# Optimization experiments

Measured on AMD Instinct MI355X. Metric: run time of the kernel, lower is better.

Reference implementation:

```python
import jax, jax.numpy as jnp
import numpy as np

T, H, E, I, K = 1024, 2048, 32, 1024, 2  # tokens, hidden, experts, intermediate (per rank), top_k


def setup_inputs() -> dict:
    key = jax.random.key(0)
    k0, k1, k2, k3 = jax.random.split(key, 4)
    s = 0.02  # weight init scale
    return {
        "hidden_states": jax.random.normal(k0, (T, H), jnp.float32),
        "w_qkv": jax.random.normal(k1, (3 * E, H), jnp.float32) * s,   # router query_key_value weight
        "w1": jax.random.normal(k2, (E, 2 * I, H), jnp.float32) * s,   # gate/up projection per expert
        "w2": jax.random.normal(k3, (E, H, I), jnp.float32) * s,       # down projection per expert
    }


def _router_logits(x, w_qkv):
    # ParallelAttention_router: per-token attention over the expert axis.
    mix = x @ w_qkv.T                      # [T, 3E]
    q, k, v = jnp.split(mix, 3, axis=-1)   # each [T, E]
    q = q.astype(jnp.float32)
    k = k.astype(jnp.float32)
    v = v.astype(jnp.float32)
    # attn[t, e, f] = softmax_f(q[t, e] * k[t, f])
    attn = jax.nn.softmax(q[:, :, None] * k[:, None, :], axis=-1)  # [T, E, E]
    return jnp.einsum('tef,tf->te', attn, v)                        # [T, E]


def reference(hidden_states, w_qkv, w1, w2):
    n_tok = hidden_states.shape[0]
    logits = _router_logits(hidden_states, w_qkv)                   # [T, E]
    top_logits, topk_ids = jax.lax.top_k(logits, K)                 # [T, K]
    topk_w = jax.nn.softmax(top_logits.astype(jnp.float32), axis=-1)  # renormalize=False -> plain softmax over top-k
    # Dense combine weights: zero for non-selected experts (honors top-k sparsity in math).
    combine = jnp.zeros((n_tok, E), jnp.float32).at[
        jnp.arange(n_tok)[:, None], topk_ids].add(topk_w)           # [T, E]
    # Expert MLP: SiLU-gated FFN (fused_experts contract: w1 -> [gate; up], w2 -> down).
    gate_up = jnp.einsum('th,eih->tei', hidden_states, w1)          # [T, E, 2I]
    gate, up = jnp.split(gate_up, 2, axis=-1)                       # each [T, E, I]
    h = jax.nn.silu(gate) * up * combine[:, :, None]                # fold combine weight in early
    out = jnp.einsum('tei,ehi->th', h, w2)                          # [T, H]
    return out.astype(hidden_states.dtype)
```

## Files before the change

kernel.cpp:

```cpp
#include <hip/hip_runtime.h>
#include <hip/hip_bf16.h>
#include <math.h>

#define TT 1024
#define HH 2048
#define EE 32
#define II 1024
#define BK2 128
#define SA2 136
#define TS2 (128 * SA2)
#define KSP 32
#define MB 64

typedef __attribute__((ext_vector_type(8))) short bf16x8;
typedef __attribute__((ext_vector_type(8))) unsigned short ushort8;
typedef __attribute__((ext_vector_type(4))) float f32x4;

__device__ __forceinline__ unsigned short f2b(float f) {
    union { float f; unsigned u; } c; c.f = f;
    unsigned r = c.u + 0x7FFFu + ((c.u >> 16) & 1u);
    return (unsigned short)(r >> 16);
}
__device__ __forceinline__ float b2f(unsigned short u) {
    union { unsigned u; float f; } c; c.u = ((unsigned)u) << 16;
    return c.f;
}
__device__ __forceinline__ unsigned cvtpk(float lo, float hi) {
    unsigned r;
    asm("v_cvt_pk_bf16_f32 %0, %1, %2" : "=v"(r) : "v"(lo), "v"(hi));
    return r;
}
__device__ __forceinline__ ushort8 pack8(float4 a, float4 b) {
    union { unsigned u[4]; ushort8 s; } cv;
    cv.u[0] = cvtpk(a.x, a.y); cv.u[1] = cvtpk(a.z, a.w);
    cv.u[2] = cvtpk(b.x, b.y); cv.u[3] = cvtpk(b.z, b.w);
    return cv.s;
}

__global__ __launch_bounds__(256) void k_cvtx(const float* __restrict__ x,
                                              unsigned short* __restrict__ xb) {
    int i = blockIdx.x * 256 + threadIdx.x;
    const float4* s = (const float4*)(x + (size_t)i * 8);
    float4 v0 = s[0], v1 = s[1];
    *(ushort8*)(xb + (size_t)i * 8) = pack8(v0, v1);
}

__global__ __launch_bounds__(256) void k_mix(const float* __restrict__ x,
                                             const float* __restrict__ wqkv,
                                             float* __restrict__ mixp) {
    __shared__ float xs[MB][68];
    __shared__ float ws_[96][68];
    const int tm0 = blockIdx.x * MB;
    const int k0 = blockIdx.y * 64;
    const int tid = threadIdx.x;
#pragma unroll
    for (int q = 0; q < 4; ++q) {
        int p = tid + q * 256;
        int row = p >> 4, c4 = (p & 15) * 4;
        *(float4*)&xs[row][c4] = *(const float4*)(x + (size_t)(tm0 + row) * HH + k0 + c4);
    }
#pragma unroll
    for (int q = 0; q < 6; ++q) {
        int p = tid + q * 256;
        int row = p >> 4, c4 = (p & 15) * 4;
        *(float4*)&ws_[row][c4] = *(const float4*)(wqkv + (size_t)row * HH + k0 + c4);
    }
    __syncthreads();
    const int tg = tid >> 4, cg = tid & 15;
    float acc[4][6];
#pragma unroll
    for (int i = 0; i < 4; ++i)
#pragma unroll
        for (int c = 0; c < 6; ++c) acc[i][c] = 0.f;
    for (int k = 0; k < 64; k += 4) {
        float4 xv[4], wv[6];
#pragma unroll
        for (int i = 0; i < 4; ++i) xv[i] = *(const float4*)&xs[tg * 4 + i][k];
#pragma unroll
        for (int c = 0; c < 6; ++c) wv[c] = *(const float4*)&ws_[cg * 6 + c][k];
#pragma unroll
        for (int i = 0; i < 4; ++i)
#pragma unroll
            for (int c = 0; c < 6; ++c)
                acc[i][c] += xv[i].x * wv[c].x + xv[i].y * wv[c].y +
                             xv[i].z * wv[c].z + xv[i].w * wv[c].w;
    }
    float* dst = mixp + ((size_t)blockIdx.y * TT + tm0) * 96;
#pragma unroll
    for (int i = 0; i < 4; ++i)
#pragma unroll
        for (int c = 0; c < 6; ++c)
            dst[(tg * 4 + i) * 96 + cg * 6 + c] = acc[i][c];
}

__global__ void k_router_attn(const float* __restrict__ mixp,
                              int* __restrict__ cnt,
                              int* __restrict__ tok_list,
                              float* __restrict__ wgt_list) {
    const int t = blockIdx.x;
    __shared__ float mrow[96];
    __shared__ float lg[EE];
    const int tid = threadIdx.x;
    if (tid < 96) {
        float s = 0.f;
        for (int sp = 0; sp < KSP; ++sp)
            s += mixp[((size_t)sp * TT + t) * 96 + tid];
        mrow[tid] = s;
    }
    __syncthreads();
    if (tid < EE) {
        float q = mrow[tid];
        float m = -1e30f;
        for (int f = 0; f < EE; ++f) m = fmaxf(m, q * mrow[32 + f]);
        float s = 0.f, a = 0.f;
        for (int f = 0; f < EE; ++f) {
            float ex = expf(q * mrow[32 + f] - m);
            s += ex;
            a += ex * mrow[64 + f];
        }
        lg[tid] = a / s;
    }
    __syncthreads();
    if (tid == 0) {
        int b0 = 0; float v0 = lg[0];
        for (int e2 = 1; e2 < EE; ++e2)
            if (lg[e2] > v0) { v0 = lg[e2]; b0 = e2; }
        int b1 = -1; float v1 = -1e30f;
        for (int e2 = 0; e2 < EE; ++e2)
            if (e2 != b0 && lg[e2] > v1) { v1 = lg[e2]; b1 = e2; }
        float ex = expf(v1 - v0);
        float w0 = 1.f / (1.f + ex);
        float w1 = ex / (1.f + ex);
        int p0 = atomicAdd(&cnt[b0], 1);
        tok_list[b0 * TT + p0] = t * 2 + 0;
        wgt_list[b0 * TT + p0] = w0;
        int p1 = atomicAdd(&cnt[b1], 1);
        tok_list[b1 * TT + p1] = t * 2 + 1;
        wgt_list[b1 * TT + p1] = w1;
    }
}

__global__ __launch_bounds__(256, 2) void k_gemm1(
    const unsigned short* __restrict__ xb, const float* __restrict__ w1,
    const int* __restrict__ cnt, const int* __restrict__ tok_list,
    const float* __restrict__ wgt_list, unsigned short* __restrict__ act) {
    const int e = blockIdx.y;
    const int M = cnt[e];
    const int m0 = blockIdx.z * 128;
    if (m0 >= M) return;
    const int i0 = blockIdx.x * 64;

    __shared__ __align__(16) unsigned short As[TS2];
    __shared__ __align__(16) unsigned short Bs[TS2];
    __shared__ int ts[128];
    __shared__ float tw[128];

    const int tid = threadIdx.x;
    if (tid < 128) {
        int mr = m0 + tid;
        if (mr < M) {
            ts[tid] = tok_list[e * TT + mr];
            tw[tid] = wgt_list[e * TT + mr];
        } else { ts[tid] = -1; tw[tid] = 0.f; }
    }
    __syncthreads();

    const float* w1e = w1 + (size_t)e * (2 * II) * HH;
    const int wid = tid >> 6;
    const int lane = tid & 63;
    const int wm = wid >> 1, wn = wid & 1;
    const int fr = lane & 15;
    const int kg = lane >> 4;
    const int srow = tid >> 4;
    const int sc8 = (tid & 15) * 8;

    f32x4 acc[4][4];
#pragma unroll
    for (int i = 0; i < 4; ++i)
#pragma unroll
        for (int j = 0; j < 4; ++j) acc[i][j] = (f32x4){0.f, 0.f, 0.f, 0.f};

    ushort8 pa8[8];
    float4 pb[16];
    const ushort8 u8z = {0, 0, 0, 0, 0, 0, 0, 0};

#define G1_LOAD(kk)                                                              \
    do {                                                                         \
        const int kkv_ = (kk);                                                   \
        _Pragma("unroll")                                                        \
        for (int q = 0; q < 8; ++q) {                                            \
            int row = q * 16 + srow;                                             \
            int entry = ts[row];                                                 \
            pa8[q] = (entry >= 0)                                                \
                ? *(const ushort8*)(xb + (size_t)(entry >> 1) * HH + kkv_ + sc8) \
                : u8z;                                                           \
            int brow = (row < 64) ? (i0 + row) : (II + i0 + row - 64);           \
            const float* gpb_ = w1e + (size_t)brow * HH + kkv_ + sc8;            \
            pb[2 * q] = ((const float4*)gpb_)[0];                                \
            pb[2 * q + 1] = ((const float4*)gpb_)[1];                            \
        }                                                                        \
    } while (0)

#define G1_CVT()                                                                 \
    do {                                                                         \
        _Pragma("unroll")                                                        \
        for (int q = 0; q < 8; ++q) {                                            \
            int row = q * 16 + srow;                                             \
            *(ushort8*)&As[row * SA2 + sc8] = pa8[q];                            \
            *(ushort8*)&Bs[row * SA2 + sc8] = pack8(pb[2 * q], pb[2 * q + 1]);   \
        }                                                                        \
    } while (0)

    const int NS = HH / BK2;
    G1_LOAD(0);
    for (int s = 0; s < NS; ++s) {
        __syncthreads();
        G1_CVT();
        __syncthreads();
        if (s + 1 < NS) G1_LOAD((s + 1) * BK2);
#pragma unroll
        for (int kh = 0; kh < 4; ++kh) {
            const int kb = kh * 32 + kg * 8;
            bf16x8 a[4], b[4];
#pragma unroll
            for (int i = 0; i < 4; ++i)
                a[i] = *(const bf16x8*)&As[(wm * 64 + i * 16 + fr) * SA2 + kb];
#pragma unroll
            for (int j = 0; j < 4; ++j)
                b[j] = *(const bf16x8*)&Bs[(wn * 64 + j * 16 + fr) * SA2 + kb];
#pragma unroll
            for (int i = 0; i < 4; ++i)
#pragma unroll
                for (int j = 0; j < 4; ++j)
                    acc[i][j] = __builtin_amdgcn_mfma_f32_16x16x32_bf16(a[i], b[j], acc[i][j], 0, 0, 0);
        }
    }
#undef G1_LOAD
#undef G1_CVT

    unsigned short* upls = As;
    __syncthreads();
    if (wn == 1) {
#pragma unroll
        for (int mi = 0; mi < 4; ++mi)
#pragma unroll
            for (int reg = 0; reg < 4; ++reg) {
                int mrow = wm * 64 + mi * 16 + kg * 4 + reg;
#pragma unroll
                for (int ni = 0; ni < 4; ++ni)
                    upls[mrow * 64 + ni * 16 + fr] = f2b(acc[mi][ni][reg]);
            }
    }
    __syncthreads();
    if (wn == 0) {
#pragma unroll
        for (int mi = 0; mi < 4; ++mi)
#pragma unroll
            for (int reg = 0; reg < 4; ++reg) {
                int mrow = wm * 64 + mi * 16 + kg * 4 + reg;
                int entry = ts[mrow];
                if (entry < 0) continue;
                float w = tw[mrow];
                unsigned short* dst = act + (size_t)entry * II + i0;
#pragma unroll
                for (int ni = 0; ni < 4; ++ni) {
                    float g = acc[mi][ni][reg];
                    float u = b2f(upls[mrow * 64 + ni * 16 + fr]);
                    dst[ni * 16 + fr] = f2b((g / (1.f + __expf(-g))) * u * w);
                }
            }
    }
}

__global__ __launch_bounds__(256, 2) void k_gemm2(
    const unsigned short* __restrict__ act, const float* __restrict__ w2,
    const int* __restrict__ cnt, const int* __restrict__ tok_list,
    float* __restrict__ po) {
    const int e = blockIdx.y;
    const int M = cnt[e];
    const int m0 = blockIdx.z * 128;
    if (m0 >= M) return;
    const int n0 = blockIdx.x * 128;

    __shared__ __align__(16) unsigned short As[TS2];
    __shared__ __align__(16) unsigned short Bs[TS2];
    __shared__ int ts[128];

    const int tid = threadIdx.x;
    if (tid < 128) {
        int mr = m0 + tid;
        ts[tid] = (mr < M) ? tok_list[e * TT + mr] : -1;
    }
    __syncthreads();

    const float* w2e = w2 + (size_t)e * HH * II;
    const int wid = tid >> 6;
    const int lane = tid & 63;
    const int wm = wid >> 1, wn = wid & 1;
    const int fr = lane & 15;
    const int kg = lane >> 4;
    const int srow = tid >> 4;
    const int sc8 = (tid & 15) * 8;

    f32x4 acc[4][4];
#pragma unroll
    for (int i = 0; i < 4; ++i)
#pragma unroll
        for (int j = 0; j < 4; ++j) acc[i][j] = (f32x4){0.f, 0.f, 0.f, 0.f};

    ushort8 pa8[8];
    float4 pb[16];
    const ushort8 u8z = {0, 0, 0, 0, 0, 0, 0, 0};

#define G2_LOAD(kk)                                                              \
    do {                                                                         \
        const int kkv_ = (kk);                                                   \
        _Pragma("unroll")                                                        \
        for (int q = 0; q < 8; ++q) {                                            \
            int row = q * 16 + srow;                                             \
            int entry = ts[row];                                                 \
            pa8[q] = (entry >= 0)                                                \
                ? *(const ushort8*)(act + (size_t)entry * II + kkv_ + sc8)       \
                : u8z;                                                           \
            const float* gpb_ = w2e + (size_t)(n0 + row) * II + kkv_ + sc8;      \
            pb[2 * q] = ((const float4*)gpb_)[0];                                \
            pb[2 * q + 1] = ((const float4*)gpb_)[1];                            \
        }                                                                        \
    } while (0)

#define G2_CVT()                                                                 \
    do {                                                                         \
        _Pragma("unroll")                                                        \
        for (int q = 0; q < 8; ++q) {                                            \
            int row = q * 16 + srow;                                             \
            *(ushort8*)&As[row * SA2 + sc8] = pa8[q];                            \
            *(ushort8*)&Bs[row * SA2 + sc8] = pack8(pb[2 * q], pb[2 * q + 1]);   \
        }                                                                        \
    } while (0)

    const int NS = II / BK2;
    G2_LOAD(0);
    for (int s = 0; s < NS; ++s) {
        __syncthreads();
        G2_CVT();
        __syncthreads();
        if (s + 1 < NS) G2_LOAD((s + 1) * BK2);
#pragma unroll
        for (int kh = 0; kh < 4; ++kh) {
            const int kb = kh * 32 + kg * 8;
            bf16x8 a[4], b[4];
#pragma unroll
            for (int i = 0; i < 4; ++i)
                a[i] = *(const bf16x8*)&As[(wm * 64 + i * 16 + fr) * SA2 + kb];
#pragma unroll
            for (int j = 0; j < 4; ++j)
                b[j] = *(const bf16x8*)&Bs[(wn * 64 + j * 16 + fr) * SA2 + kb];
#pragma unroll
            for (int i = 0; i < 4; ++i)
#pragma unroll
                for (int j = 0; j < 4; ++j)
                    acc[i][j] = __builtin_amdgcn_mfma_f32_16x16x32_bf16(a[i], b[j], acc[i][j], 0, 0, 0);
        }
    }
#undef G2_LOAD
#undef G2_CVT

#pragma unroll
    for (int mi = 0; mi < 4; ++mi) {
#pragma unroll
        for (int reg = 0; reg < 4; ++reg) {
            int m = wm * 64 + mi * 16 + kg * 4 + reg;
            int entry = ts[m];
            if (entry < 0) continue;
            float* op = po + (size_t)entry * HH + n0 + wn * 64;
#pragma unroll
            for (int ni = 0; ni < 4; ++ni)
                op[ni * 16 + fr] = acc[mi][ni][reg];
        }
    }
}

__global__ __launch_bounds__(256) void k_combine(const float* __restrict__ po,
                                                 float* __restrict__ out) {
    int i = blockIdx.x * 256 + threadIdx.x;
    int t = i / (HH / 4);
    int c = i % (HH / 4);
    float4 a = ((const float4*)(po + (size_t)(2 * t) * HH))[c];
    float4 b = ((const float4*)(po + (size_t)(2 * t + 1) * HH))[c];
    float4 r = make_float4(a.x + b.x, a.y + b.y, a.z + b.z, a.w + b.w);
    ((float4*)(out + (size_t)t * HH))[c] = r;
}

extern "C" void kernel_launch(void* const* d_in, const int* in_sizes, int n_in,
                              void* d_out, int out_size, void* d_ws, size_t ws_size,
                              hipStream_t stream) {
    const float* x    = (const float*)d_in[0];
    const float* wqkv = (const float*)d_in[1];
    const float* w1   = (const float*)d_in[2];
    const float* w2   = (const float*)d_in[3];
    float* out = (float*)d_out;

    char* ws = (char*)d_ws;
    float* mixp           = (float*)(ws);
    float* wgt_list       = (float*)(ws + 12582912);
    int*   tok_list       = (int*)  (ws + 12713984);
    int*   cnt            = (int*)  (ws + 12845056);
    unsigned short* xb    = (unsigned short*)(ws + 12845184);
    unsigned short* act   = (unsigned short*)(ws + 17039488);
    float* po             = (float*)(ws + 21233792);

    (void)hipMemsetAsync(cnt, 0, 128, stream);

    k_cvtx<<<TT * HH / 8 / 256, 256, 0, stream>>>(x, xb);
    k_mix<<<dim3(TT / MB, KSP), 256, 0, stream>>>(x, wqkv, mixp);
    k_router_attn<<<TT, 128, 0, stream>>>(mixp, cnt, tok_list, wgt_list);
    k_gemm1<<<dim3(II / 64, EE, 8), 256, 0, stream>>>(xb, w1, cnt, tok_list, wgt_list, act);
    k_gemm2<<<dim3(HH / 128, EE, 8), 256, 0, stream>>>(act, w2, cnt, tok_list, po);
    k_combine<<<TT * HH / 4 / 256, 256, 0, stream>>>(po, out);
}
```

Baseline: 220.1 us.

## Loop over M tiles inside GEMM blocks and swizzle expert/N block mapping

Both expert GEMM kernels now launch one block per (expert, N-tile) instead of one per (expert, N-tile, M-tile). Each block loops over all 128-row M tiles of its expert, and the block index is swizzled so that neighbouring blocks cover different experts. This removes thousands of blocks that only exited early and spreads concurrent work across experts. The cost is that experts with many tokens are processed serially within one block, which can cause load imbalance.

New measurement: 248.8 us. 1.13x slower.

```diff
diff --git a/kernel.cpp b/kernel.cpp
--- a/kernel.cpp
+++ b/kernel.cpp
@@ -140,15 +140,20 @@
     }
 }
 
+__device__ __forceinline__ void swz_en(int lin, int& e, int& n) {
+    int r = lin & 7, q = lin >> 3;
+    e = r + 8 * (q >> 4);
+    n = q & 15;
+}
+
 __global__ __launch_bounds__(256, 2) void k_gemm1(
     const unsigned short* __restrict__ xb, const float* __restrict__ w1,
     const int* __restrict__ cnt, const int* __restrict__ tok_list,
     const float* __restrict__ wgt_list, unsigned short* __restrict__ act) {
-    const int e = blockIdx.y;
+    int e, nblk;
+    swz_en(blockIdx.y * 16 + blockIdx.x, e, nblk);
     const int M = cnt[e];
-    const int m0 = blockIdx.z * 128;
-    if (m0 >= M) return;
-    const int i0 = blockIdx.x * 64;
+    const int i0 = nblk * 64;
 
     __shared__ __align__(16) unsigned short As[TS2];
     __shared__ __align__(16) unsigned short Bs[TS2];
@@ -156,15 +161,6 @@
     __shared__ float tw[128];
 
     const int tid = threadIdx.x;
-    if (tid < 128) {
-        int mr = m0 + tid;
-        if (mr < M) {
-            ts[tid] = tok_list[e * TT + mr];
-            tw[tid] = wgt_list[e * TT + mr];
-        } else { ts[tid] = -1; tw[tid] = 0.f; }
-    }
-    __syncthreads();
-
     const float* w1e = w1 + (size_t)e * (2 * II) * HH;
     const int wid = tid >> 6;
     const int lane = tid & 63;
@@ -174,15 +170,26 @@
     const int srow = tid >> 4;
     const int sc8 = (tid & 15) * 8;
 
-    f32x4 acc[4][4];
-#pragma unroll
-    for (int i = 0; i < 4; ++i)
-#pragma unroll
-        for (int j = 0; j < 4; ++j) acc[i][j] = (f32x4){0.f, 0.f, 0.f, 0.f};
-
     ushort8 pa8[8];
     float4 pb[16];
     const ushort8 u8z = {0, 0, 0, 0, 0, 0, 0, 0};
+
+    for (int m0 = 0; m0 < M; m0 += 128) {
+        __syncthreads();
+        if (tid < 128) {
+            int mr = m0 + tid;
+            if (mr < M) {
+                ts[tid] = tok_list[e * TT + mr];
+                tw[tid] = wgt_list[e * TT + mr];
+            } else { ts[tid] = -1; tw[tid] = 0.f; }
+        }
+        __syncthreads();
+
+        f32x4 acc[4][4];
+#pragma unroll
+        for (int i = 0; i < 4; ++i)
+#pragma unroll
+            for (int j = 0; j < 4; ++j) acc[i][j] = (f32x4){0.f, 0.f, 0.f, 0.f};
 
 #define G1_LOAD(kk)                                                              \
     do {                                                                         \
@@ -211,64 +218,65 @@
         }                                                                        \
     } while (0)
 
-    const int NS = HH / BK2;
-    G1_LOAD(0);
-    for (int s = 0; s < NS; ++s) {
-        __syncthreads();
-        G1_CVT();
-        __syncthreads();
-        if (s + 1 < NS) G1_LOAD((s + 1) * BK2);
-#pragma unroll
-        for (int kh = 0; kh < 4; ++kh) {
-            const int kb = kh * 32 + kg * 8;
-            bf16x8 a[4], b[4];
-#pragma unroll
-            for (int i = 0; i < 4; ++i)
-                a[i] = *(const bf16x8*)&As[(wm * 64 + i * 16 + fr) * SA2 + kb];
-#pragma unroll
-            for (int j = 0; j < 4; ++j)
-                b[j] = *(const bf16x8*)&Bs[(wn * 64 + j * 16 + fr) * SA2 + kb];
-#pragma unroll
-            for (int i = 0; i < 4; ++i)
+        const int NS = HH / BK2;
+        G1_LOAD(0);
+        for (int s = 0; s < NS; ++s) {
+            __syncthreads();
+            G1_CVT();
+            __syncthreads();
+            if (s + 1 < NS) G1_LOAD((s + 1) * BK2);
+#pragma unroll
+            for (int kh = 0; kh < 4; ++kh) {
+                const int kb = kh * 32 + kg * 8;
+                bf16x8 a[4], b[4];
+#pragma unroll
+                for (int i = 0; i < 4; ++i)
+                    a[i] = *(const bf16x8*)&As[(wm * 64 + i * 16 + fr) * SA2 + kb];
 #pragma unroll
                 for (int j = 0; j < 4; ++j)
-                    acc[i][j] = __builtin_amdgcn_mfma_f32_16x16x32_bf16(a[i], b[j], acc[i][j], 0, 0, 0);
-        }
-    }
+                    b[j] = *(const bf16x8*)&Bs[(wn * 64 + j * 16 + fr) * SA2 + kb];
+#pragma unroll
+                for (int i = 0; i < 4; ++i)
+#pragma unroll
+                    for (int j = 0; j < 4; ++j)
+                        acc[i][j] = __builtin_amdgcn_mfma_f32_16x16x32_bf16(a[i], b[j], acc[i][j], 0, 0, 0);
+            }
+        }
 #undef G1_LOAD
 #undef G1_CVT
 
-    unsigned short* upls = As;
-    __syncthreads();
-    if (wn == 1) {
-#pragma unroll
-        for (int mi = 0; mi < 4; ++mi)
-#pragma unroll
-            for (int reg = 0; reg < 4; ++reg) {
-                int mrow = wm * 64 + mi * 16 + kg * 4 + reg;
-#pragma unroll
-                for (int ni = 0; ni < 4; ++ni)
-                    upls[mrow * 64 + ni * 16 + fr] = f2b(acc[mi][ni][reg]);
-            }
-    }
-    __syncthreads();
-    if (wn == 0) {
-#pragma unroll
-        for (int mi = 0; mi < 4; ++mi)
-#pragma unroll
-            for (int reg = 0; reg < 4; ++reg) {
-                int mrow = wm * 64 + mi * 16 + kg * 4 + reg;
-                int entry = ts[mrow];
-                if (entry < 0) continue;
-                float w = tw[mrow];
-                unsigned short* dst = act + (size_t)entry * II + i0;
-#pragma unroll
-                for (int ni = 0; ni < 4; ++ni) {
-                    float g = acc[mi][ni][reg];
-                    float u = b2f(upls[mrow * 64 + ni * 16 + fr]);
-                    dst[ni * 16 + fr] = f2b((g / (1.f + __expf(-g))) * u * w);
+        unsigned short* upls = As;
+        __syncthreads();
+        if (wn == 1) {
+#pragma unroll
+            for (int mi = 0; mi < 4; ++mi)
+#pragma unroll
+                for (int reg = 0; reg < 4; ++reg) {
+                    int mrow = wm * 64 + mi * 16 + kg * 4 + reg;
+#pragma unroll
+                    for (int ni = 0; ni < 4; ++ni)
+                        upls[mrow * 64 + ni * 16 + fr] = f2b(acc[mi][ni][reg]);
                 }
-            }
+        }
+        __syncthreads();
+        if (wn == 0) {
+#pragma unroll
+            for (int mi = 0; mi < 4; ++mi)
+#pragma unroll
+                for (int reg = 0; reg < 4; ++reg) {
+                    int mrow = wm * 64 + mi * 16 + kg * 4 + reg;
+                    int entry = ts[mrow];
+                    if (entry < 0) continue;
+                    float w = tw[mrow];
+                    unsigned short* dst = act + (size_t)entry * II + i0;
+#pragma unroll
+                    for (int ni = 0; ni < 4; ++ni) {
+                        float g = acc[mi][ni][reg];
+                        float u = b2f(upls[mrow * 64 + ni * 16 + fr]);
+                        dst[ni * 16 + fr] = f2b((g / (1.f + __expf(-g))) * u * w);
+                    }
+                }
+        }
     }
 }
 
@@ -276,23 +284,16 @@
     const unsigned short* __restrict__ act, const float* __restrict__ w2,
     const int* __restrict__ cnt, const int* __restrict__ tok_list,
     float* __restrict__ po) {
-    const int e = blockIdx.y;
+    int e, nblk;
+    swz_en(blockIdx.y * 16 + blockIdx.x, e, nblk);
     const int M = cnt[e];
-    const int m0 = blockIdx.z * 128;
-    if (m0 >= M) return;
-    const int n0 = blockIdx.x * 128;
+    const int n0 = nblk * 128;
 
     __shared__ __align__(16) unsigned short As[TS2];
     __shared__ __align__(16) unsigned short Bs[TS2];
     __shared__ int ts[128];
 
     const int tid = threadIdx.x;
-    if (tid < 128) {
-        int mr = m0 + tid;
-        ts[tid] = (mr < M) ? tok_list[e * TT + mr] : -1;
-    }
-    __syncthreads();
-
     const float* w2e = w2 + (size_t)e * HH * II;
     const int wid = tid >> 6;
     const int lane = tid & 63;
@@ -302,15 +303,23 @@
     const int srow = tid >> 4;
     const int sc8 = (tid & 15) * 8;
 
-    f32x4 acc[4][4];
-#pragma unroll
-    for (int i = 0; i < 4; ++i)
-#pragma unroll
-        for (int j = 0; j < 4; ++j) acc[i][j] = (f32x4){0.f, 0.f, 0.f, 0.f};
-
     ushort8 pa8[8];
     float4 pb[16];
     const ushort8 u8z = {0, 0, 0, 0, 0, 0, 0, 0};
+
+    for (int m0 = 0; m0 < M; m0 += 128) {
+        __syncthreads();
+        if (tid < 128) {
+            int mr = m0 + tid;
+            ts[tid] = (mr < M) ? tok_list[e * TT + mr] : -1;
+        }
+        __syncthreads();
+
+        f32x4 acc[4][4];
+#pragma unroll
+        for (int i = 0; i < 4; ++i)
+#pragma unroll
+            for (int j = 0; j < 4; ++j) acc[i][j] = (f32x4){0.f, 0.f, 0.f, 0.f};
 
 #define G2_LOAD(kk)                                                              \
     do {                                                                         \
@@ -338,45 +347,47 @@
         }                                                                        \
     } while (0)
 
-    const int NS = II / BK2;
-    G2_LOAD(0);
-    for (int s = 0; s < NS; ++s) {
-        __syncthreads();
-        G2_CVT();
-        __syncthreads();
-        if (s + 1 < NS) G2_LOAD((s + 1) * BK2);
-#pragma unroll
-        for (int kh = 0; kh < 4; ++kh) {
-            const int kb = kh * 32 + kg * 8;
-            bf16x8 a[4], b[4];
-#pragma unroll
-            for (int i = 0; i < 4; ++i)
-                a[i] = *(const bf16x8*)&As[(wm * 64 + i * 16 + fr) * SA2 + kb];
-#pragma unroll
-            for (int j = 0; j < 4; ++j)
-                b[j] = *(const bf16x8*)&Bs[(wn * 64 + j * 16 + fr) * SA2 + kb];
-#pragma unroll
-            for (int i = 0; i < 4; ++i)
+        const int NS = II / BK2;
+        G2_LOAD(0);
+        for (int s = 0; s < NS; ++s) {
+            __syncthreads();
+            G2_CVT();
+            __syncthreads();
+            if (s + 1 < NS) G2_LOAD((s + 1) * BK2);
+#pragma unroll
+            for (int kh = 0; kh < 4; ++kh) {
+                const int kb = kh * 32 + kg * 8;
+                bf16x8 a[4], b[4];
+#pragma unroll
+                for (int i = 0; i < 4; ++i)
+                    a[i] = *(const bf16x8*)&As[(wm * 64 + i * 16 + fr) * SA2 + kb];
 #pragma unroll
                 for (int j = 0; j < 4; ++j)
-                    acc[i][j] = __builtin_amdgcn_mfma_f32_16x16x32_bf16(a[i], b[j], acc[i][j], 0, 0, 0);
-        }
-    }
+                    b[j] = *(const bf16x8*)&Bs[(wn * 64 + j * 16 + fr) * SA2 + kb];
+#pragma unroll
+                for (int i = 0; i < 4; ++i)
+#pragma unroll
+                    for (int j = 0; j < 4; ++j)
+                        acc[i][j] = __builtin_amdgcn_mfma_f32_16x16x32_bf16(a[i], b[j], acc[i][j], 0, 0, 0);
+            }
+        }
 #undef G2_LOAD
 #undef G2_CVT
 
 #pragma unroll
-    for (int mi = 0; mi < 4; ++mi) {
-#pragma unroll
-        for (int reg = 0; reg < 4; ++reg) {
-            int m = wm * 64 + mi * 16 + kg * 4 + reg;
-            int entry = ts[m];
-            if (entry < 0) continue;
-            float* op = po + (size_t)entry * HH + n0 + wn * 64;
-#pragma unroll
-            for (int ni = 0; ni < 4; ++ni)
-                op[ni * 16 + fr] = acc[mi][ni][reg];
-        }
+        for (int mi = 0; mi < 4; ++mi) {
+#pragma unroll
+            for (int reg = 0; reg < 4; ++reg) {
+                int m = wm * 64 + mi * 16 + kg * 4 + reg;
+                int entry = ts[m];
+                if (entry < 0) continue;
+                float* op = po + (size_t)entry * HH + n0 + wn * 64;
+#pragma unroll
+                for (int ni = 0; ni < 4; ++ni)
+                    op[ni * 16 + fr] = acc[mi][ni][reg];
+            }
+        }
+        __syncthreads();
     }
 }
 
@@ -414,7 +425,7 @@
     k_cvtx<<<TT * HH / 8 / 256, 256, 0, stream>>>(x, xb);
     k_mix<<<dim3(TT / MB, KSP), 256, 0, stream>>>(x, wqkv, mixp);
     k_router_attn<<<TT, 128, 0, stream>>>(mixp, cnt, tok_list, wgt_list);
-    k_gemm1<<<dim3(II / 64, EE, 8), 256, 0, stream>>>(xb, w1, cnt, tok_list, wgt_list, act);
-    k_gemm2<<<dim3(HH / 128, EE, 8), 256, 0, stream>>>(act, w2, cnt, tok_list, po);
+    k_gemm1<<<dim3(16, EE), 256, 0, stream>>>(xb, w1, cnt, tok_list, wgt_list, act);
+    k_gemm2<<<dim3(16, EE), 256, 0, stream>>>(act, w2, cnt, tok_list, po);
     k_combine<<<TT * HH / 4 / 256, 256, 0, stream>>>(po, out);
 }
```
